# Kernel optimization log

Measured on AMD Instinct MI355X. Metric: run time of the kernel, lower is better.

The kernel has to match this reference:

```python
import jax, jax.numpy as jnp
import numpy as np
import math

B, S, D, H = 8, 1024, 1024, 16
HD = D // H
MAX_LEN = 1024

def setup_inputs() -> dict:
    key = jax.random.key(0)
    ks = jax.random.split(key, 16)
    s = 1.0 / math.sqrt(D)
    return {
        "query": jax.random.normal(ks[0], (B, S, D), jnp.float32),
        "key_in": jax.random.normal(ks[1], (B, S, D), jnp.float32),
        "value": jax.random.normal(ks[2], (B, S, D), jnp.float32),
        "mask": jax.random.randint(ks[3], (B, S, S), 0, 2, jnp.int32),
        "Wq": jax.random.normal(ks[4], (D, D), jnp.float32) * s,
        "bq": jnp.zeros((D,), jnp.float32),
        "Wk": jax.random.normal(ks[5], (D, D), jnp.float32) * s,
        "bk": jnp.zeros((D,), jnp.float32),
        "Wv": jax.random.normal(ks[6], (D, D), jnp.float32) * s,
        "bv": jnp.zeros((D,), jnp.float32),
        "Wo": jax.random.normal(ks[7], (D, D), jnp.float32) * s,
        "bo": jnp.zeros((D,), jnp.float32),
        "syn_scores": jax.random.normal(ks[8], (H, MAX_LEN, MAX_LEN), jnp.float32) * 0.02,
        "alpha_param": jax.random.normal(ks[9], (1,), jnp.float32),
    }

def reference(query, key_in, value, mask, Wq, bq, Wk, bk, Wv, bv, Wo, bo, syn_scores, alpha_param):
    b, s, d = query.shape
    # projections (torch Linear: x @ W.T + b), split heads -> [b,h,s,hd]
    q = (query @ Wq.T + bq).reshape(b, s, H, HD).transpose(0, 2, 1, 3)
    k = (key_in @ Wk.T + bk).reshape(b, s, H, HD).transpose(0, 2, 1, 3)
    v = (value @ Wv.T + bv).reshape(b, s, H, HD).transpose(0, 2, 1, 3)
    scores = jnp.einsum("bhqd,bhkd->bhqk", q, k) / jnp.sqrt(jnp.float32(HD))
    # synthesizer scores: slice (seq_len <= max_sent_len path; equal-len matches torch)
    syn = syn_scores[:, :s, :s]  # [h,s,s]
    alpha = jax.nn.sigmoid(alpha_param)[0]
    merged = scores * alpha + (1.0 - alpha) * syn[None]
    merged = jnp.where(mask[:, None] == 0, jnp.float32(-1e9), merged)
    attn = jax.nn.softmax(merged, axis=-1)  # dropout disabled (eval)
    out = jnp.einsum("bhqk,bhkd->bhqd", attn, v)
    out = out.transpose(0, 2, 1, 3).reshape(b, s, d)
    return out @ Wo.T + bo
```

## Files before the change

### kernel.cpp

```cpp
#include <hip/hip_runtime.h>
#include <stdint.h>

#define BB 8
#define SS 1024
#define DD 1024
#define HH 16
#define HDIM 64

typedef _Float16 half8 __attribute__((ext_vector_type(8)));
typedef _Float16 half4 __attribute__((ext_vector_type(4)));
typedef float   float4v __attribute__((ext_vector_type(4)));
typedef float   float8v __attribute__((ext_vector_type(8)));

#define AS1(p) ((__attribute__((address_space(1))) void*)(p))
#define AS3(p) ((__attribute__((address_space(3))) void*)(p))

#define LOG2E 1.4426950408889634f

#if __has_builtin(__builtin_amdgcn_exp2f)
#define EXP2(x) __builtin_amdgcn_exp2f(x)
#else
#define EXP2(x) __expf((x) * 0.6931471805599453f)
#endif

struct CvtArgs {
    const float* src[6];
    _Float16*    dst[6];
    long long    n[6];
    int          scaled[6];
    const float* alp;
};

__global__ __launch_bounds__(256) void cvt_f32_f16(CvtArgs a) {
    int seg = blockIdx.y;
    long long base = ((long long)blockIdx.x * 256 + threadIdx.x) * 8;
    if (base >= a.n[seg]) return;
    float s = 1.0f;
    if (a.scaled[seg]) s = (1.0f - 1.0f / (1.0f + __expf(-a.alp[0]))) * LOG2E;
    float8v u = *(const float8v*)(a.src[seg] + base);
    half8 h;
#pragma unroll
    for (int i = 0; i < 8; ++i) h[i] = (_Float16)(u[i] * s);
    *(half8*)(a.dst[seg] + base) = h;
}

__global__ __launch_bounds__(256) void pack_mask(const int* __restrict__ mask,
                                                 unsigned long long* __restrict__ bits) {
    long long gid = (long long)blockIdx.x * 256 + threadIdx.x;
    int m = mask[gid];
    unsigned long long bal = __ballot(m != 0);
    if ((threadIdx.x & 63) == 0) bits[gid >> 6] = bal;
}

template <int MODE, bool SCALEQ>
__global__ __launch_bounds__(256) void gemm_bt(
    const _Float16* __restrict__ A,
    const _Float16* __restrict__ W,
    const float* __restrict__ bias,
    void* __restrict__ out,
    const float* __restrict__ alp)
{
    constexpr int K = 1024, BM = 128, BK = 64;
    __shared__ _Float16 As[BM * BK];
    __shared__ _Float16 Bs[BM * BK];

    const int tid  = threadIdx.x;
    const int lane = tid & 63;
    const int wave = tid >> 6;
    const int wm = wave >> 1, wn = wave & 1;
    const int m0 = blockIdx.x * BM;
    const int n0 = blockIdx.y * BM;

    float4v acc[4][4] = {};

    for (int kt = 0; kt < K; kt += BK) {
#pragma unroll
        for (int i = 0; i < 4; ++i) {
            int flat = ((wave * 4 + i) * 64 + lane) * 8;
            int r = flat >> 6, c = flat & 63;
            const _Float16* ga = A + (long long)(m0 + r) * K + kt + c;
            const _Float16* gb = W + (long long)(n0 + r) * K + kt + c;
            __builtin_amdgcn_global_load_lds(AS1(ga), AS3(&As[flat]), 16, 0, 0);
            __builtin_amdgcn_global_load_lds(AS1(gb), AS3(&Bs[flat]), 16, 0, 0);
        }
        __syncthreads();
#pragma unroll
        for (int kk = 0; kk < BK; kk += 32) {
            half8 af[4], bf[4];
#pragma unroll
            for (int t = 0; t < 4; ++t) {
                af[t] = *(const half8*)&As[(wm * 64 + t * 16 + (lane & 15)) * BK + kk + (lane >> 4) * 8];
                bf[t] = *(const half8*)&Bs[(wn * 64 + t * 16 + (lane & 15)) * BK + kk + (lane >> 4) * 8];
            }
#pragma unroll
            for (int mt = 0; mt < 4; ++mt)
#pragma unroll
                for (int nt = 0; nt < 4; ++nt)
                    acc[mt][nt] = __builtin_amdgcn_mfma_f32_16x16x32_f16(af[mt], bf[nt], acc[mt][nt], 0, 0, 0);
        }
        __syncthreads();
    }

    float qscale = 1.0f;
    if constexpr (SCALEQ) qscale = 0.125f * LOG2E / (1.0f + __expf(-alp[0]));

#pragma unroll
    for (int mt = 0; mt < 4; ++mt) {
#pragma unroll
        for (int nt = 0; nt < 4; ++nt) {
            int n  = n0 + wn * 64 + nt * 16 + (lane & 15);
            int mb = m0 + wm * 64 + mt * 16 + (lane >> 4) * 4;
            float bn = bias[n];
            if constexpr (MODE == 0) {
                _Float16* o = (_Float16*)out;
                int b = mb >> 10, s = mb & 1023, h = n >> 6, hd = n & 63;
                long long idx = ((long long)(b * 16 + h) * 1024 + s) * 64 + hd;
#pragma unroll
                for (int i = 0; i < 4; ++i)
                    o[idx + (long long)i * 64] = (_Float16)((acc[mt][nt][i] + bn) * qscale);
            } else if constexpr (MODE == 1) {
                _Float16* o = (_Float16*)out;
                int b = mb >> 10, s = mb & 1023, h = n >> 6, hd = n & 63;
                long long tbase = (((long long)(b * 16 + h)) * 16 + (s >> 6)) * 4096;
                int off = ((hd * 128 + (s & 63) * 2) ^ ((hd & 15) << 3)) >> 1;
                half4 hv;
#pragma unroll
                for (int i = 0; i < 4; ++i) hv[i] = (_Float16)(acc[mt][nt][i] + bn);
                *(half4*)&o[tbase + off] = hv;
            } else if constexpr (MODE == 3) {
                _Float16* o = (_Float16*)out;
                int b = mb >> 10, s = mb & 1023, h = n >> 6, hd = n & 63;
                long long tbase = (((long long)(b * 16 + h)) * 16 + (s >> 6)) * 4096;
#pragma unroll
                for (int i = 0; i < 4; ++i) {
                    int key = (s & 63) + i;
                    o[tbase + (((key * 128 + hd * 2) ^ ((key & 7) << 4)) >> 1)] =
                        (_Float16)(acc[mt][nt][i] + bn);
                }
            } else {
                float* o = (float*)out;
#pragma unroll
                for (int i = 0; i < 4; ++i)
                    o[(long long)(mb + i) * 1024 + n] = acc[mt][nt][i] + bn;
            }
        }
    }
}

__global__ __launch_bounds__(256) void attn_kernel(
    const _Float16* __restrict__ qw,
    const _Float16* __restrict__ ktl,
    const _Float16* __restrict__ vtl,
    const unsigned long long* __restrict__ mbits,
    const _Float16* __restrict__ synh,
    _Float16* __restrict__ ao)
{
    __shared__ __align__(16) _Float16 KsA[4096];
    __shared__ __align__(16) _Float16 VsA[4096];
    __shared__ __align__(16) _Float16 KsB[4096];
    __shared__ __align__(16) _Float16 VsB[4096];

    const int tid  = threadIdx.x;
    const int lane = tid & 63;
    const int wave = tid >> 6;
    const int bid  = ((blockIdx.x & 7) << 7) | (blockIdx.x >> 3);
    const int b  = bid >> 7;
    const int h  = (bid >> 3) & 15;
    const int q0 = (bid & 7) * 128 + wave * 32;
    const int bh = b * 16 + h;

    half8 qf[2][2];
#pragma unroll
    for (int f = 0; f < 2; ++f) {
        const _Float16* qb = qw + ((long long)bh * SS + q0 + f * 16 + (lane & 15)) * HDIM + (lane >> 4) * 8;
        qf[f][0] = *(const half8*)qb;
        qf[f][1] = *(const half8*)(qb + 32);
    }

    float4v o[2][4] = {};
    float4v ol[2]   = {};
    float mrun[2] = {-3e38f, -3e38f};

    const _Float16* kgb = ktl + (long long)bh * 16 * 4096;
    const _Float16* vgb = vtl + (long long)bh * 16 * 4096;
    const unsigned long long* mb0 = mbits + ((long long)b * SS + q0 + (lane & 15)) * 16;
    const _Float16* syn0 = synh + ((long long)h * SS + q0 + (lane & 15)) * SS + ((lane >> 4) << 2);
    const _Float16* syn1 = syn0 + 16 * (long long)SS;

    const int tid8 = tid * 8;

    const int kswz = (lane & 7) << 4;
    const int kb0h = (((((lane & 15) << 7) + ((lane >> 4) << 4))      ) ^ kswz) >> 1;
    const int kb1h = (((((lane & 15) << 7) + ((lane >> 4) << 4)) + 64 ) ^ kswz) >> 1;
    int vbh[4];
#pragma unroll
    for (int ks = 0; ks < 4; ++ks)
        vbh[ks] = ((((lane & 15) << 7) + ks * 32 + ((lane >> 4) << 3)) ^ ((lane & 15) << 3)) >> 1;

    auto stage = [&](_Float16* Ksb, _Float16* Vsb, int t) {
        const _Float16* kg = kgb + t * 4096 + tid8;
        const _Float16* vg = vgb + t * 4096 + tid8;
        __builtin_amdgcn_global_load_lds(AS1(kg),        AS3(Ksb + tid8),        16, 0, 0);
        __builtin_amdgcn_global_load_lds(AS1(kg + 2048), AS3(Ksb + tid8 + 2048), 16, 0, 0);
        __builtin_amdgcn_global_load_lds(AS1(vg),        AS3(Vsb + tid8),        16, 0, 0);
        __builtin_amdgcn_global_load_lds(AS1(vg + 2048), AS3(Vsb + tid8 + 2048), 16, 0, 0);
    };

    half4 svA[2][4], svB[2][4];
    unsigned long long btA[2], btB[2];

    auto loadSyn = [&](int t, half4 (&sv)[2][4], unsigned long long (&bt)[2]) {
        bt[0] = mb0[t];
        bt[1] = mb0[256 + t];
        const int kb = t << 6;
#pragma unroll
        for (int ks = 0; ks < 4; ++ks) {
            sv[0][ks] = *(const half4*)(syn0 + kb + ks * 16);
            sv[1][ks] = *(const half4*)(syn1 + kb + ks * 16);
        }
    };

    const half4 vone = {(_Float16)1.f, (_Float16)1.f, (_Float16)1.f, (_Float16)1.f};

    auto compute = [&](const _Float16 (&Ks)[4096], const _Float16 (&Vs)[4096],
                       half4 (&sv)[2][4], unsigned long long (&bt)[2]) {
        float4v st[2][4];
#pragma unroll
        for (int ks = 0; ks < 4; ++ks) {
            half8 k0 = *(const half8*)&Ks[kb0h + ks * 1024];
            half8 k1 = *(const half8*)&Ks[kb1h + ks * 1024];
#pragma unroll
            for (int f = 0; f < 2; ++f) {
                float4v s;
#pragma unroll
                for (int i = 0; i < 4; ++i) s[i] = (float)sv[f][ks][i];
                s = __builtin_amdgcn_mfma_f32_16x16x32_f16(k0, qf[f][0], s, 0, 0, 0);
                s = __builtin_amdgcn_mfma_f32_16x16x32_f16(k1, qf[f][1], s, 0, 0, 0);
                st[f][ks] = s;
            }
        }
        half4 pf[2][4];
#pragma unroll
        for (int f = 0; f < 2; ++f) {
            const unsigned long long bits = bt[f];
            float tmax = -3e38f;
#pragma unroll
            for (int ks = 0; ks < 4; ++ks)
#pragma unroll
                for (int i = 0; i < 4; ++i) {
                    int pos = ks * 16 + ((lane >> 4) << 2) + i;
                    float sc = ((bits >> pos) & 1ull) ? st[f][ks][i] : -1e9f;
                    st[f][ks][i] = sc;
                    tmax = fmaxf(tmax, sc);
                }
            tmax = fmaxf(tmax, __shfl_xor(tmax, 16));
            tmax = fmaxf(tmax, __shfl_xor(tmax, 32));
            if (__any(tmax > mrun[f] + 8.0f)) {
                float mnew = fmaxf(mrun[f], tmax);
                float corr = EXP2(mrun[f] - mnew);
                float cr[4];
#pragma unroll
                for (int i = 0; i < 4; ++i) cr[i] = __shfl(corr, ((lane >> 4) << 2) + i);
#pragma unroll
                for (int n = 0; n < 4; ++n)
#pragma unroll
                    for (int i = 0; i < 4; ++i) o[f][n][i] *= cr[i];
#pragma unroll
                for (int i = 0; i < 4; ++i) ol[f][i] *= cr[i];
                mrun[f] = mnew;
            }
#pragma unroll
            for (int ks = 0; ks < 4; ++ks)
#pragma unroll
                for (int i = 0; i < 4; ++i)
                    pf[f][ks][i] = (_Float16)EXP2(st[f][ks][i] - mrun[f]);
        }
#pragma unroll
        for (int ks = 0; ks < 4; ++ks) {
            ol[0] = __builtin_amdgcn_mfma_f32_16x16x16f16(pf[0][ks], vone, ol[0], 0, 0, 0);
            ol[1] = __builtin_amdgcn_mfma_f32_16x16x16f16(pf[1][ks], vone, ol[1], 0, 0, 0);
#pragma unroll
            for (int n = 0; n < 4; ++n) {
                half4 vf = *(const half4*)&Vs[vbh[ks] + n * 1024];
                o[0][n] = __builtin_amdgcn_mfma_f32_16x16x16f16(pf[0][ks], vf, o[0][n], 0, 0, 0);
                o[1][n] = __builtin_amdgcn_mfma_f32_16x16x16f16(pf[1][ks], vf, o[1][n], 0, 0, 0);
            }
        }
    };

    stage(KsA, VsA, 0);
    loadSyn(0, svA, btA);
    __syncthreads();

    for (int t = 0; t < 16; t += 2) {
        stage(KsB, VsB, t + 1);
        loadSyn(t + 1, svB, btB);
        compute(KsA, VsA, svA, btA);
        __syncthreads();
        if (t + 2 < 16) {
            stage(KsA, VsA, t + 2);
            loadSyn(t + 2, svA, btA);
        }
        compute(KsB, VsB, svB, btB);
        __syncthreads();
    }

#pragma unroll
    for (int f = 0; f < 2; ++f) {
        float inv[4];
#pragma unroll
        for (int i = 0; i < 4; ++i) inv[i] = 1.0f / ol[f][i];
#pragma unroll
        for (int n = 0; n < 4; ++n)
#pragma unroll
            for (int i = 0; i < 4; ++i) {
                int qrow = q0 + f * 16 + (lane >> 4) * 4 + i;
                long long idx = ((long long)b * SS + qrow) * DD + h * 64 + n * 16 + (lane & 15);
                ao[idx] = (_Float16)(o[f][n][i] * inv[i]);
            }
    }
}

extern "C" void kernel_launch(void* const* d_in, const int* in_sizes, int n_in,
                              void* d_out, int out_size, void* d_ws, size_t ws_size,
                              hipStream_t stream) {
    const float* query  = (const float*)d_in[0];
    const float* key_in = (const float*)d_in[1];
    const float* value  = (const float*)d_in[2];
    const int*   mask   = (const int*)d_in[3];
    const float* Wq = (const float*)d_in[4];
    const float* bq = (const float*)d_in[5];
    const float* Wk = (const float*)d_in[6];
    const float* bk = (const float*)d_in[7];
    const float* Wv = (const float*)d_in[8];
    const float* bv = (const float*)d_in[9];
    const float* Wo = (const float*)d_in[10];
    const float* bo = (const float*)d_in[11];
    const float* syn = (const float*)d_in[12];
    const float* alp = (const float*)d_in[13];

    const long long XN = (long long)BB * SS * DD;
    const long long WN = (long long)DD * DD;
    const long long SN = (long long)HH * SS * SS;

    _Float16* ws   = (_Float16*)d_ws;
    _Float16* xbuf = ws;
    _Float16* wqf  = ws + XN;
    _Float16* wkf  = wqf + WN;
    _Float16* wvf  = wkf + WN;
    _Float16* wof  = wvf + WN;
    _Float16* qws  = wof + WN;
    _Float16* kws  = qws + XN;
    _Float16* vTws = kws + XN;
    _Float16* synh = vTws + XN;
    unsigned long long* mbits = (unsigned long long*)(synh + SN);
    _Float16* ao   = xbuf;

    dim3 blk(256);
    dim3 ggrid(64, 8);

    CvtArgs a1;
    a1.src[0] = query;  a1.dst[0] = xbuf; a1.n[0] = XN; a1.scaled[0] = 0;
    a1.src[1] = Wq;     a1.dst[1] = wqf;  a1.n[1] = WN; a1.scaled[1] = 0;
    a1.src[2] = Wk;     a1.dst[2] = wkf;  a1.n[2] = WN; a1.scaled[2] = 0;
    a1.src[3] = Wv;     a1.dst[3] = wvf;  a1.n[3] = WN; a1.scaled[3] = 0;
    a1.src[4] = Wo;     a1.dst[4] = wof;  a1.n[4] = WN; a1.scaled[4] = 0;
    a1.src[5] = syn;    a1.dst[5] = synh; a1.n[5] = SN; a1.scaled[5] = 1;
    a1.alp = alp;
    cvt_f32_f16<<<dim3(8192, 6), blk, 0, stream>>>(a1);

    pack_mask<<<dim3(32768), blk, 0, stream>>>(mask, mbits);

    gemm_bt<0, true><<<ggrid, blk, 0, stream>>>(xbuf, wqf, bq, qws, alp);

    CvtArgs a2 = a1; a2.src[0] = key_in;
    cvt_f32_f16<<<dim3(4096, 1), blk, 0, stream>>>(a2);
    gemm_bt<3, false><<<ggrid, blk, 0, stream>>>(xbuf, wkf, bk, kws, alp);

    CvtArgs a3 = a1; a3.src[0] = value;
    cvt_f32_f16<<<dim3(4096, 1), blk, 0, stream>>>(a3);
    gemm_bt<1, false><<<ggrid, blk, 0, stream>>>(xbuf, wvf, bv, vTws, alp);

    attn_kernel<<<dim3(1024), blk, 0, stream>>>(qws, kws, vTws, mbits, synh, ao);

    gemm_bt<2, false><<<ggrid, blk, 0, stream>>>(ao, wof, bo, d_out, alp);
}
```

Before: 473.4 us.

## Double-buffer GEMM LDS tiles and batch Q/K/V projections into one launch

```diff
diff --git a/kernel.cpp b/kernel.cpp
--- a/kernel.cpp
+++ b/kernel.cpp
@@ -24,24 +24,29 @@
 #endif
 
 struct CvtArgs {
-    const float* src[6];
-    _Float16*    dst[6];
-    long long    n[6];
-    int          scaled[6];
+    const float* src[8];
+    _Float16*    dst[8];
+    long long    n[8];
+    int          scaled[8];
     const float* alp;
 };
 
 __global__ __launch_bounds__(256) void cvt_f32_f16(CvtArgs a) {
-    int seg = blockIdx.y;
-    long long base = ((long long)blockIdx.x * 256 + threadIdx.x) * 8;
-    if (base >= a.n[seg]) return;
+    const int seg = blockIdx.y;
+    const long long n = a.n[seg];
     float s = 1.0f;
     if (a.scaled[seg]) s = (1.0f - 1.0f / (1.0f + __expf(-a.alp[0]))) * LOG2E;
-    float8v u = *(const float8v*)(a.src[seg] + base);
-    half8 h;
-#pragma unroll
-    for (int i = 0; i < 8; ++i) h[i] = (_Float16)(u[i] * s);
-    *(half8*)(a.dst[seg] + base) = h;
+    const float* __restrict__ src = a.src[seg];
+    _Float16* __restrict__ dst = a.dst[seg];
+    const long long stride = (long long)gridDim.x * 2048;
+    for (long long base = ((long long)blockIdx.x * 256 + threadIdx.x) * 8;
+         base < n; base += stride) {
+        float8v u = *(const float8v*)(src + base);
+        half8 h;
+#pragma unroll
+        for (int i = 0; i < 8; ++i) h[i] = (_Float16)(u[i] * s);
+        *(half8*)(dst + base) = h;
+    }
 }
 
 __global__ __launch_bounds__(256) void pack_mask(const int* __restrict__ mask,
@@ -52,18 +57,70 @@
     if ((threadIdx.x & 63) == 0) bits[gid >> 6] = bal;
 }
 
-template <int MODE, bool SCALEQ>
-__global__ __launch_bounds__(256) void gemm_bt(
-    const _Float16* __restrict__ A,
-    const _Float16* __restrict__ W,
-    const float* __restrict__ bias,
-    void* __restrict__ out,
-    const float* __restrict__ alp)
+__device__ __forceinline__ void gemm_core(
+    const _Float16* __restrict__ A, const _Float16* __restrict__ W,
+    int m0, int n0, int wave, int lane, int wm, int wn,
+    _Float16* As0, _Float16* Bs0, _Float16* As1, _Float16* Bs1,
+    float4v (&acc)[4][4])
 {
-    constexpr int K = 1024, BM = 128, BK = 64;
-    __shared__ _Float16 As[BM * BK];
-    __shared__ _Float16 Bs[BM * BK];
-
+    constexpr int K = 1024, BK = 64;
+
+    auto stage = [&](_Float16* Asb, _Float16* Bsb, int kt) {
+#pragma unroll
+        for (int i = 0; i < 4; ++i) {
+            int flat = ((wave * 4 + i) * 64 + lane) * 8;
+            int r = flat >> 6, c = flat & 63;
+            const _Float16* ga = A + (long long)(m0 + r) * K + kt + c;
+            const _Float16* gb = W + (long long)(n0 + r) * K + kt + c;
+            __builtin_amdgcn_global_load_lds(AS1(ga), AS3(Asb + flat), 16, 0, 0);
+            __builtin_amdgcn_global_load_lds(AS1(gb), AS3(Bsb + flat), 16, 0, 0);
+        }
+    };
+
+    auto compute = [&](const _Float16* Asb, const _Float16* Bsb) {
+#pragma unroll
+        for (int kk = 0; kk < BK; kk += 32) {
+            half8 af[4], bf[4];
+#pragma unroll
+            for (int t = 0; t < 4; ++t) {
+                af[t] = *(const half8*)&Asb[(wm * 64 + t * 16 + (lane & 15)) * BK + kk + (lane >> 4) * 8];
+                bf[t] = *(const half8*)&Bsb[(wn * 64 + t * 16 + (lane & 15)) * BK + kk + (lane >> 4) * 8];
+            }
+#pragma unroll
+            for (int mt = 0; mt < 4; ++mt)
+#pragma unroll
+                for (int nt = 0; nt < 4; ++nt)
+                    acc[mt][nt] = __builtin_amdgcn_mfma_f32_16x16x32_f16(af[mt], bf[nt], acc[mt][nt], 0, 0, 0);
+        }
+    };
+
+    stage(As0, Bs0, 0);
+    __syncthreads();
+    for (int kt = 0; kt < K; kt += 2 * BK) {
+        stage(As1, Bs1, kt + BK);
+        compute(As0, Bs0);
+        __syncthreads();
+        if (kt + 2 * BK < K) stage(As0, Bs0, kt + 2 * BK);
+        compute(As1, Bs1);
+        __syncthreads();
+    }
+}
+
+struct QkvArgs {
+    const _Float16* A[3];
+    const _Float16* W[3];
+    const float*    bias[3];
+    _Float16*       out[3];
+    int             mode[3];
+    const float*    alp;
+};
+
+__global__ __launch_bounds__(256) void gemm_qkv(QkvArgs g) {
+    constexpr int BM = 128, BK = 64;
+    __shared__ _Float16 As0[BM * BK], Bs0[BM * BK];
+    __shared__ _Float16 As1[BM * BK], Bs1[BM * BK];
+
+    const int z = blockIdx.z;
     const int tid  = threadIdx.x;
     const int lane = tid & 63;
     const int wave = tid >> 6;
@@ -72,37 +129,13 @@
     const int n0 = blockIdx.y * BM;
 
     float4v acc[4][4] = {};
-
-    for (int kt = 0; kt < K; kt += BK) {
-#pragma unroll
-        for (int i = 0; i < 4; ++i) {
-            int flat = ((wave * 4 + i) * 64 + lane) * 8;
-            int r = flat >> 6, c = flat & 63;
-            const _Float16* ga = A + (long long)(m0 + r) * K + kt + c;
-            const _Float16* gb = W + (long long)(n0 + r) * K + kt + c;
-            __builtin_amdgcn_global_load_lds(AS1(ga), AS3(&As[flat]), 16, 0, 0);
-            __builtin_amdgcn_global_load_lds(AS1(gb), AS3(&Bs[flat]), 16, 0, 0);
-        }
-        __syncthreads();
-#pragma unroll
-        for (int kk = 0; kk < BK; kk += 32) {
-            half8 af[4], bf[4];
-#pragma unroll
-            for (int t = 0; t < 4; ++t) {
-                af[t] = *(const half8*)&As[(wm * 64 + t * 16 + (lane & 15)) * BK + kk + (lane >> 4) * 8];
-                bf[t] = *(const half8*)&Bs[(wn * 64 + t * 16 + (lane & 15)) * BK + kk + (lane >> 4) * 8];
-            }
-#pragma unroll
-            for (int mt = 0; mt < 4; ++mt)
-#pragma unroll
-                for (int nt = 0; nt < 4; ++nt)
-                    acc[mt][nt] = __builtin_amdgcn_mfma_f32_16x16x32_f16(af[mt], bf[nt], acc[mt][nt], 0, 0, 0);
-        }
-        __syncthreads();
-    }
-
+    gemm_core(g.A[z], g.W[z], m0, n0, wave, lane, wm, wn, As0, Bs0, As1, Bs1, acc);
+
+    const int mode = g.mode[z];
     float qscale = 1.0f;
-    if constexpr (SCALEQ) qscale = 0.125f * LOG2E / (1.0f + __expf(-alp[0]));
+    if (mode == 0) qscale = 0.125f * LOG2E / (1.0f + __expf(-g.alp[0]));
+    _Float16* o = g.out[z];
+    const float* bias = g.bias[z];
 
 #pragma unroll
     for (int mt = 0; mt < 4; ++mt) {
@@ -111,38 +144,62 @@
             int n  = n0 + wn * 64 + nt * 16 + (lane & 15);
             int mb = m0 + wm * 64 + mt * 16 + (lane >> 4) * 4;
             float bn = bias[n];
-            if constexpr (MODE == 0) {
-                _Float16* o = (_Float16*)out;
-                int b = mb >> 10, s = mb & 1023, h = n >> 6, hd = n & 63;
-                long long idx = ((long long)(b * 16 + h) * 1024 + s) * 64 + hd;
+            int b = mb >> 10, sI = mb & 1023, hI = n >> 6, hd = n & 63;
+            if (mode == 0) {
+                long long idx = ((long long)(b * 16 + hI) * 1024 + sI) * 64 + hd;
 #pragma unroll
                 for (int i = 0; i < 4; ++i)
                     o[idx + (long long)i * 64] = (_Float16)((acc[mt][nt][i] + bn) * qscale);
-            } else if constexpr (MODE == 1) {
-                _Float16* o = (_Float16*)out;
-                int b = mb >> 10, s = mb & 1023, h = n >> 6, hd = n & 63;
-                long long tbase = (((long long)(b * 16 + h)) * 16 + (s >> 6)) * 4096;
-                int off = ((hd * 128 + (s & 63) * 2) ^ ((hd & 15) << 3)) >> 1;
-                half4 hv;
-#pragma unroll
-                for (int i = 0; i < 4; ++i) hv[i] = (_Float16)(acc[mt][nt][i] + bn);
-                *(half4*)&o[tbase + off] = hv;
-            } else if constexpr (MODE == 3) {
-                _Float16* o = (_Float16*)out;
-                int b = mb >> 10, s = mb & 1023, h = n >> 6, hd = n & 63;
-                long long tbase = (((long long)(b * 16 + h)) * 16 + (s >> 6)) * 4096;
+            } else if (mode == 1) {
+                long long tbase = (((long long)(b * 16 + hI)) * 16 + (sI >> 6)) * 4096;
 #pragma unroll
                 for (int i = 0; i < 4; ++i) {
-                    int key = (s & 63) + i;
+                    int key = (sI & 63) + i;
                     o[tbase + (((key * 128 + hd * 2) ^ ((key & 7) << 4)) >> 1)] =
                         (_Float16)(acc[mt][nt][i] + bn);
                 }
             } else {
-                float* o = (float*)out;
-#pragma unroll
-                for (int i = 0; i < 4; ++i)
-                    o[(long long)(mb + i) * 1024 + n] = acc[mt][nt][i] + bn;
-            }
+                long long tbase = (((long long)(b * 16 + hI)) * 16 + (sI >> 6)) * 4096;
+                int off = ((hd * 128 + (sI & 63) * 2) ^ ((hd & 15) << 3)) >> 1;
+                half4 hv;
+#pragma unroll
+                for (int i = 0; i < 4; ++i) hv[i] = (_Float16)(acc[mt][nt][i] + bn);
+                *(half4*)&o[tbase + off] = hv;
+            }
+        }
+    }
+}
+
+__global__ __launch_bounds__(256) void gemm_o(
+    const _Float16* __restrict__ A,
+    const _Float16* __restrict__ W,
+    const float* __restrict__ bias,
+    float* __restrict__ out)
+{
+    constexpr int BM = 128, BK = 64;
+    __shared__ _Float16 As0[BM * BK], Bs0[BM * BK];
+    __shared__ _Float16 As1[BM * BK], Bs1[BM * BK];
+
+    const int tid  = threadIdx.x;
+    const int lane = tid & 63;
+    const int wave = tid >> 6;
+    const int wm = wave >> 1, wn = wave & 1;
+    const int m0 = blockIdx.x * BM;
+    const int n0 = blockIdx.y * BM;
+
+    float4v acc[4][4] = {};
+    gemm_core(A, W, m0, n0, wave, lane, wm, wn, As0, Bs0, As1, Bs1, acc);
+
+#pragma unroll
+    for (int mt = 0; mt < 4; ++mt) {
+#pragma unroll
+        for (int nt = 0; nt < 4; ++nt) {
+            int n  = n0 + wn * 64 + nt * 16 + (lane & 15);
+            int mb = m0 + wm * 64 + mt * 16 + (lane >> 4) * 4;
+            float bn = bias[n];
+#pragma unroll
+            for (int i = 0; i < 4; ++i)
+                out[(long long)(mb + i) * 1024 + n] = acc[mt][nt][i] + bn;
         }
     }
 }
@@ -343,45 +400,91 @@
     const long long WN = (long long)DD * DD;
     const long long SN = (long long)HH * SS * SS;
 
-    _Float16* ws   = (_Float16*)d_ws;
-    _Float16* xbuf = ws;
-    _Float16* wqf  = ws + XN;
-    _Float16* wkf  = wqf + WN;
-    _Float16* wvf  = wkf + WN;
-    _Float16* wof  = wvf + WN;
-    _Float16* qws  = wof + WN;
-    _Float16* kws  = qws + XN;
-    _Float16* vTws = kws + XN;
-    _Float16* synh = vTws + XN;
-    unsigned long long* mbits = (unsigned long long*)(synh + SN);
-    _Float16* ao   = xbuf;
-
+    _Float16* ws = (_Float16*)d_ws;
     dim3 blk(256);
     dim3 ggrid(64, 8);
 
-    CvtArgs a1;
-    a1.src[0] = query;  a1.dst[0] = xbuf; a1.n[0] = XN; a1.scaled[0] = 0;
-    a1.src[1] = Wq;     a1.dst[1] = wqf;  a1.n[1] = WN; a1.scaled[1] = 0;
-    a1.src[2] = Wk;     a1.dst[2] = wkf;  a1.n[2] = WN; a1.scaled[2] = 0;
-    a1.src[3] = Wv;     a1.dst[3] = wvf;  a1.n[3] = WN; a1.scaled[3] = 0;
-    a1.src[4] = Wo;     a1.dst[4] = wof;  a1.n[4] = WN; a1.scaled[4] = 0;
-    a1.src[5] = syn;    a1.dst[5] = synh; a1.n[5] = SN; a1.scaled[5] = 1;
-    a1.alp = alp;
-    cvt_f32_f16<<<dim3(8192, 6), blk, 0, stream>>>(a1);
-
-    pack_mask<<<dim3(32768), blk, 0, stream>>>(mask, mbits);
-
-    gemm_bt<0, true><<<ggrid, blk, 0, stream>>>(xbuf, wqf, bq, qws, alp);
-
-    CvtArgs a2 = a1; a2.src[0] = key_in;
-    cvt_f32_f16<<<dim3(4096, 1), blk, 0, stream>>>(a2);
-    gemm_bt<3, false><<<ggrid, blk, 0, stream>>>(xbuf, wkf, bk, kws, alp);
-
-    CvtArgs a3 = a1; a3.src[0] = value;
-    cvt_f32_f16<<<dim3(4096, 1), blk, 0, stream>>>(a3);
-    gemm_bt<1, false><<<ggrid, blk, 0, stream>>>(xbuf, wvf, bv, vTws, alp);
-
-    attn_kernel<<<dim3(1024), blk, 0, stream>>>(qws, kws, vTws, mbits, synh, ao);
-
-    gemm_bt<2, false><<<ggrid, blk, 0, stream>>>(ao, wof, bo, d_out, alp);
-}
+    if (ws_size >= ((size_t)140 << 20)) {
+        _Float16* qx   = ws;
+        _Float16* kx   = qx + XN;
+        _Float16* vx   = kx + XN;
+        _Float16* wqf  = vx + XN;
+        _Float16* wkf  = wqf + WN;
+        _Float16* wvf  = wkf + WN;
+        _Float16* wof  = wvf + WN;
+        _Float16* qws  = wof + WN;
+        _Float16* kws  = qws + XN;
+        _Float16* vTws = kws + XN;
+        _Float16* synh = vTws + XN;
+        unsigned long long* mbits = (unsigned long long*)(synh + SN);
+        _Float16* ao = qx;
+
+        CvtArgs a = {};
+        a.src[0] = query;  a.dst[0] = qx;   a.n[0] = XN; a.scaled[0] = 0;
+        a.src[1] = key_in; a.dst[1] = kx;   a.n[1] = XN; a.scaled[1] = 0;
+        a.src[2] = value;  a.dst[2] = vx;   a.n[2] = XN; a.scaled[2] = 0;
+        a.src[3] = Wq;     a.dst[3] = wqf;  a.n[3] = WN; a.scaled[3] = 0;
+        a.src[4] = Wk;     a.dst[4] = wkf;  a.n[4] = WN; a.scaled[4] = 0;
+        a.src[5] = Wv;     a.dst[5] = wvf;  a.n[5] = WN; a.scaled[5] = 0;
+        a.src[6] = Wo;     a.dst[6] = wof;  a.n[6] = WN; a.scaled[6] = 0;
+        a.src[7] = syn;    a.dst[7] = synh; a.n[7] = SN; a.scaled[7] = 1;
+        a.alp = alp;
+        cvt_f32_f16<<<dim3(2048, 8), blk, 0, stream>>>(a);
+
+        pack_mask<<<dim3(32768), blk, 0, stream>>>(mask, mbits);
+
+        QkvArgs g;
+        g.A[0] = qx;  g.W[0] = wqf; g.bias[0] = bq; g.out[0] = qws;  g.mode[0] = 0;
+        g.A[1] = kx;  g.W[1] = wkf; g.bias[1] = bk; g.out[1] = kws;  g.mode[1] = 1;
+        g.A[2] = vx;  g.W[2] = wvf; g.bias[2] = bv; g.out[2] = vTws; g.mode[2] = 2;
+        g.alp = alp;
+        gemm_qkv<<<dim3(64, 8, 3), blk, 0, stream>>>(g);
+
+        attn_kernel<<<dim3(1024), blk, 0, stream>>>(qws, kws, vTws, mbits, synh, ao);
+
+        gemm_o<<<ggrid, blk, 0, stream>>>(ao, wof, bo, (float*)d_out);
+    } else {
+        _Float16* xbuf = ws;
+        _Float16* wqf  = ws + XN;
+        _Float16* wkf  = wqf + WN;
+        _Float16* wvf  = wkf + WN;
+        _Float16* wof  = wvf + WN;
+        _Float16* qws  = wof + WN;
+        _Float16* kws  = qws + XN;
+        _Float16* vTws = kws + XN;
+        _Float16* synh = vTws + XN;
+        unsigned long long* mbits = (unsigned long long*)(synh + SN);
+        _Float16* ao = xbuf;
+
+        CvtArgs a1 = {};
+        a1.src[0] = query; a1.dst[0] = xbuf; a1.n[0] = XN; a1.scaled[0] = 0;
+        a1.src[1] = Wq;    a1.dst[1] = wqf;  a1.n[1] = WN; a1.scaled[1] = 0;
+        a1.src[2] = Wk;    a1.dst[2] = wkf;  a1.n[2] = WN; a1.scaled[2] = 0;
+        a1.src[3] = Wv;    a1.dst[3] = wvf;  a1.n[3] = WN; a1.scaled[3] = 0;
+        a1.src[4] = Wo;    a1.dst[4] = wof;  a1.n[4] = WN; a1.scaled[4] = 0;
+        a1.src[5] = syn;   a1.dst[5] = synh; a1.n[5] = SN; a1.scaled[5] = 1;
+        a1.alp = alp;
+        cvt_f32_f16<<<dim3(2048, 6), blk, 0, stream>>>(a1);
+
+        pack_mask<<<dim3(32768), blk, 0, stream>>>(mask, mbits);
+
+        QkvArgs g;
+        g.alp = alp;
+        g.A[0] = xbuf; g.W[0] = wqf; g.bias[0] = bq; g.out[0] = qws; g.mode[0] = 0;
+        gemm_qkv<<<dim3(64, 8, 1), blk, 0, stream>>>(g);
+
+        CvtArgs a2 = a1; a2.src[0] = key_in;
+        cvt_f32_f16<<<dim3(2048, 1), blk, 0, stream>>>(a2);
+        g.A[0] = xbuf; g.W[0] = wkf; g.bias[0] = bk; g.out[0] = kws; g.mode[0] = 1;
+        gemm_qkv<<<dim3(64, 8, 1), blk, 0, stream>>>(g);
+
+        CvtArgs a3 = a1; a3.src[0] = value;
+        cvt_f32_f16<<<dim3(2048, 1), blk, 0, stream>>>(a3);
+        g.A[0] = xbuf; g.W[0] = wvf; g.bias[0] = bv; g.out[0] = vTws; g.mode[0] = 2;
+        gemm_qkv<<<dim3(64, 8, 1), blk, 0, stream>>>(g);
+
+        attn_kernel<<<dim3(1024), blk, 0, stream>>>(qws, kws, vTws, mbits, synh, ao);
+
+        gemm_o<<<ggrid, blk, 0, stream>>>(ao, wof, bo, (float*)d_out);
+    }
+}
```

New measurement: 465.7 us. Within noise of the previous version (-1.6%).
